# Kernel tuning notes

Hardware: AMD Instinct MI355X
Metric: run time of the kernel (lower is better)

Reference implementation:

```python
import jax, jax.numpy as jnp
import numpy as np

C = 2048
RED = 8
D = C // RED  # 256


def setup_inputs() -> dict:
    key = jax.random.key(0)
    ks = jax.random.split(key, 8)
    n, h, w = 4, 64, 64
    x = jax.random.normal(ks[0], (n, C, h, w), dtype=jnp.float32)
    # 1x1 conv weights stored as [out_ch, in_ch]
    w1 = jax.random.normal(ks[1], (D, C), dtype=jnp.float32) * 0.02
    b1 = jnp.zeros((D,), dtype=jnp.float32)
    w2 = jax.random.normal(ks[2], (D, C), dtype=jnp.float32) * 0.02
    b2 = jnp.zeros((D,), dtype=jnp.float32)
    w3 = jax.random.normal(ks[3], (C, C), dtype=jnp.float32) * 0.02
    b3 = jnp.zeros((C,), dtype=jnp.float32)
    alpha = jnp.zeros((1,), dtype=jnp.float32)
    return {"x": x, "w1": w1, "b1": b1, "w2": w2, "b2": b2,
            "w3": w3, "b3": b3, "alpha": alpha}


def reference(x, w1, b1, w2, b2, w3, b3, alpha):
    n, c, h, w = x.shape
    hw = h * w
    xf = x.reshape(n, c, hw)  # [n, C, HW]
    # 1x1 convs == per-position matmuls over channels
    e1 = jax.nn.relu(jnp.einsum('dc,ncp->ndp', w1, xf) + b1[None, :, None])  # [n, D, HW]
    e2 = jax.nn.relu(jnp.einsum('dc,ncp->ndp', w2, xf) + b2[None, :, None])  # [n, D, HW]
    assembly = jax.nn.relu(jnp.einsum('oc,ncp->nop', w3, xf) + b3[None, :, None])  # [n, C, HW]
    # attention[i, j] = softmax_j( e1[:, i] . e2[:, j] )
    scores = jnp.einsum('ndi,ndj->nij', e1, e2)  # [n, HW, HW]
    attn = jax.nn.softmax(scores, axis=-1)
    # torch.bmm(x, attn^T): out[:, :, i] = sum_j x[:, :, j] * attn[i, j]
    out = jnp.einsum('ncj,nij->nci', xf, attn)  # [n, C, HW]
    y = alpha[0] * out + assembly
    return y.reshape(n, c, h, w)
```

## Files before the change

### kernel.cpp

```cpp
#include <hip/hip_runtime.h>
#include <math.h>

#define CC 2048
#define DD 256
#define PP 4096
#define NB 4

typedef float f32x4 __attribute__((ext_vector_type(4)));
typedef __bf16 bfrag __attribute__((ext_vector_type(8)));

#define AS1(p) ((const __attribute__((address_space(1))) void*)(p))
#define AS3(p) ((__attribute__((address_space(3))) void*)(p))

__device__ __forceinline__ unsigned short f2bf(float f) {
    unsigned int u = __float_as_uint(f);
    u = (u + 0x7fffu + ((u >> 16) & 1u)) >> 16;
    return (unsigned short)u;
}

__global__ __launch_bounds__(256) void prep(const float* __restrict__ x, unsigned short* __restrict__ xT,
                                            const float* __restrict__ w3, unsigned short* __restrict__ w3b) {
    const int t = threadIdx.x;
    if (blockIdx.z == NB) {
        int bid = blockIdx.y * 64 + blockIdx.x;
        int base = (bid * 256 + t) * 8;
#pragma unroll
        for (int j = 0; j < 2; ++j) {
            float4 v = *(const float4*)(w3 + base + j * 4);
            ushort4 r;
            r.x = f2bf(v.x); r.y = f2bf(v.y); r.z = f2bf(v.z); r.w = f2bf(v.w);
            *(ushort4*)(w3b + base + j * 4) = r;
        }
        return;
    }
    __shared__ float tile[64 * 64];
    const int n  = blockIdx.z;
    const int c0 = blockIdx.y * 64;
    const int p0 = blockIdx.x * 64;
    const float* xn = x + (size_t)n * CC * PP;
    {
        const int cl = t >> 4;
        const int g  = t & 15;
        const int pl = g * 4;
#pragma unroll
        for (int ps = 0; ps < 4; ++ps) {
            const int c = cl + ps * 16;
            float4 v = *(const float4*)(xn + (size_t)(c0 + c) * PP + p0 + pl);
            const int gs = g ^ (c >> 2);
            *(float4*)(tile + c * 64 + gs * 4) = v;
        }
    }
    __syncthreads();
    unsigned short* xTn = xT + (size_t)n * PP * CC;
    {
        const int pl2 = t >> 4;
        const int cq  = t & 15;
        const int c4  = cq * 4;
#pragma unroll
        for (int ps = 0; ps < 4; ++ps) {
            const int p  = pl2 + ps * 16;
            const int gs2 = (p >> 2) ^ cq;
            const int base = gs2 * 4 + (p & 3);
            ushort4 r;
            r.x = f2bf(tile[(c4 + 0) * 64 + base]);
            r.y = f2bf(tile[(c4 + 1) * 64 + base]);
            r.z = f2bf(tile[(c4 + 2) * 64 + base]);
            r.w = f2bf(tile[(c4 + 3) * 64 + base]);
            *(ushort4*)(xTn + (size_t)(p0 + p) * CC + c0 + c4) = r;
        }
    }
}

__global__ __launch_bounds__(512, 2) void gemm_assembly(
    const unsigned short* __restrict__ w3b,
    const unsigned short* __restrict__ xT,
    const float* __restrict__ b3,
    float* __restrict__ out)
{
    __shared__ __align__(16) char sm[131072];

    const int t    = threadIdx.x;
    const int wave = t >> 6;
    const int lane = t & 63;
    const int swz  = lane & 7;

    const int p0 = blockIdx.x << 8;
    const int m0 = blockIdx.y << 8;
    const int nb = blockIdx.z;

    const int rA = t >> 3;
    const int g  = (t & 7) ^ (rA & 7);
    const unsigned short* Ag = w3b + (size_t)(m0 + rA) * CC + g * 8;
    const unsigned short* Bg = xT + (size_t)nb * PP * CC + (size_t)(p0 + rA) * CC + g * 8;
    const int ldsw = wave << 10;

    const char* Abase = sm + ((wave >> 2) << 14) + (lane & 15) * 128;
    const char* Bbase = sm + 65536 + (((wave & 3) >> 1) << 14) + ((wave & 1) << 13) + (lane & 15) * 128;

    const int ck0 = (((lane >> 4) ^ swz) << 4);
    const int ck1 = ck0 ^ 0x40;

    f32x4 acc[8][4];
#pragma unroll
    for (int i = 0; i < 8; ++i)
#pragma unroll
        for (int j = 0; j < 4; ++j)
            acc[i][j] = (f32x4){0.f, 0.f, 0.f, 0.f};

    bfrag a0k0, a0k1, a1k0, a1k1, a2k0, a2k1, a3k0, a3k1;
    bfrag a4k0, a4k1, a5k0, a5k1, a6k0, a6k1, a7k0, a7k1;
    bfrag bP0, bP1, bP2, bP3;
    bfrag bQ0, bQ1, bQ2, bQ3;

#define STG(SB, DO, kt, h) do { \
    const unsigned short* _s = (SB) + (size_t)(h) * 128 * CC + (size_t)(kt) * 64; \
    char* _d = sm + (DO) + (((kt) & 1) << 15) + ((h) << 14) + ldsw; \
    __builtin_amdgcn_global_load_lds(AS1(_s), AS3(_d), 16, 0, 0); \
    __builtin_amdgcn_global_load_lds(AS1(_s + 64 * CC), AS3(_d + 8192), 16, 0, 0); \
} while (0)

#define LD(dst, BASE, OFF) dst = *(const bfrag*)((BASE) + (OFF))
#define Q(I, J, A_, B_) acc[I][J] = __builtin_amdgcn_mfma_f32_16x16x32_bf16(A_, B_, acc[I][J], 0, 0, 0)
#define BARR __builtin_amdgcn_s_barrier()
#define SB0  __builtin_amdgcn_sched_barrier(0)
#define WLG(N) do { asm volatile("s_waitcnt lgkmcnt(" #N ")" ::: "memory"); __builtin_amdgcn_sched_barrier(0); } while (0)
#define WVM(N) asm volatile("s_waitcnt vmcnt(" #N ")" ::: "memory")
#define PRI(x) __builtin_amdgcn_s_setprio(x)

#define TILE(P, NP, kt, IA, IB, IR, V2, V0, G3, S10,S11,S12,S13, S20,S21,S22,S23) do { \
     \
    BARR; SB0; \
    LD(S20, Bbase, ((P) << 15) + (2 << 11) + ck0); LD(S21, Bbase, ((P) << 15) + (2 << 11) + ck1); \
    LD(S22, Bbase, ((P) << 15) + (3 << 11) + ck0); LD(S23, Bbase, ((P) << 15) + (3 << 11) + ck1); \
    if (IA) STG(Ag, 0, (kt) + 1, 0); \
    SB0; WLG(4); PRI(1); \
    Q(0, 0, a0k0, S10); Q(1, 0, a1k0, S10); Q(2, 0, a2k0, S10); Q(3, 0, a3k0, S10); \
    Q(0, 1, a0k0, S12); Q(1, 1, a1k0, S12); Q(2, 1, a2k0, S12); Q(3, 1, a3k0, S12); \
    Q(0, 0, a0k1, S11); Q(1, 0, a1k1, S11); Q(2, 0, a2k1, S11); Q(3, 0, a3k1, S11); \
    Q(0, 1, a0k1, S13); Q(1, 1, a1k1, S13); Q(2, 1, a2k1, S13); Q(3, 1, a3k1, S13); \
    PRI(0); \
     \
    BARR; SB0; \
    LD(a4k0, Abase, ((P) << 15) + (4 << 11) + ck0); LD(a4k1, Abase, ((P) << 15) + (4 << 11) + ck1); \
    LD(a5k0, Abase, ((P) << 15) + (5 << 11) + ck0); LD(a5k1, Abase, ((P) << 15) + (5 << 11) + ck1); \
    LD(a6k0, Abase, ((P) << 15) + (6 << 11) + ck0); LD(a6k1, Abase, ((P) << 15) + (6 << 11) + ck1); \
    LD(a7k0, Abase, ((P) << 15) + (7 << 11) + ck0); LD(a7k1, Abase, ((P) << 15) + (7 << 11) + ck1); \
    if (IA) STG(Ag, 0, (kt) + 1, 1); \
    SB0; WLG(8); PRI(1); \
    Q(0, 2, a0k0, S20); Q(1, 2, a1k0, S20); Q(2, 2, a2k0, S20); Q(3, 2, a3k0, S20); \
    Q(0, 3, a0k0, S22); Q(1, 3, a1k0, S22); Q(2, 3, a2k0, S22); Q(3, 3, a3k0, S22); \
    Q(0, 2, a0k1, S21); Q(1, 2, a1k1, S21); Q(2, 2, a2k1, S21); Q(3, 2, a3k1, S21); \
    Q(0, 3, a0k1, S23); Q(1, 3, a1k1, S23); Q(2, 3, a2k1, S23); Q(3, 3, a3k1, S23); \
    PRI(0); \
     \
     \
    BARR; SB0; \
    if (IB) STG(Bg, 65536, (kt) + 2, 0); \
    if (V2) WVM(2); \
    if (V0) WVM(0); \
    BARR; SB0; \
    if (IR) { \
        LD(a0k0, Abase, ((NP) << 15) + (0 << 11) + ck0); LD(a0k1, Abase, ((NP) << 15) + (0 << 11) + ck1); \
        LD(a1k0, Abase, ((NP) << 15) + (1 << 11) + ck0); LD(a1k1, Abase, ((NP) << 15) + (1 << 11) + ck1); \
        LD(a2k0, Abase, ((NP) << 15) + (2 << 11) + ck0); LD(a2k1, Abase, ((NP) << 15) + (2 << 11) + ck1); \
        LD(a3k0, Abase, ((NP) << 15) + (3 << 11) + ck0); LD(a3k1, Abase, ((NP) << 15) + (3 << 11) + ck1); \
    } \
    SB0; WLG(G3); PRI(1); \
    Q(4, 2, a4k0, S20); Q(5, 2, a5k0, S20); Q(6, 2, a6k0, S20); Q(7, 2, a7k0, S20); \
    Q(4, 3, a4k0, S22); Q(5, 3, a5k0, S22); Q(6, 3, a6k0, S22); Q(7, 3, a7k0, S22); \
    Q(4, 2, a4k1, S21); Q(5, 2, a5k1, S21); Q(6, 2, a6k1, S21); Q(7, 2, a7k1, S21); \
    Q(4, 3, a4k1, S23); Q(5, 3, a5k1, S23); Q(6, 3, a6k1, S23); Q(7, 3, a7k1, S23); \
    PRI(0); \
     \
    if (IB) STG(Bg, 65536, (kt) + 2, 1); \
    if (IR) { \
        LD(S20, Bbase, ((NP) << 15) + (0 << 11) + ck0); LD(S21, Bbase, ((NP) << 15) + (0 << 11) + ck1); \
        LD(S22, Bbase, ((NP) << 15) + (1 << 11) + ck0); LD(S23, Bbase, ((NP) << 15) + (1 << 11) + ck1); \
    } \
    SB0; PRI(1); \
    Q(4, 0, a4k0, S10); Q(5, 0, a5k0, S10); Q(6, 0, a6k0, S10); Q(7, 0, a7k0, S10); \
    Q(4, 1, a4k0, S12); Q(5, 1, a5k0, S12); Q(6, 1, a6k0, S12); Q(7, 1, a7k0, S12); \
    Q(4, 0, a4k1, S11); Q(5, 0, a5k1, S11); Q(6, 0, a6k1, S11); Q(7, 0, a7k1, S11); \
    Q(4, 1, a4k1, S13); Q(5, 1, a5k1, S13); Q(6, 1, a6k1, S13); Q(7, 1, a7k1, S13); \
    PRI(0); \
} while (0)

    STG(Ag, 0, 0, 0); STG(Ag, 0, 0, 1);
    STG(Bg, 65536, 0, 0); STG(Bg, 65536, 0, 1);
    STG(Bg, 65536, 1, 0); STG(Bg, 65536, 1, 1);
    WVM(4);
    BARR; SB0;
    LD(a0k0, Abase, (0 << 11) + ck0); LD(a0k1, Abase, (0 << 11) + ck1);
    LD(a1k0, Abase, (1 << 11) + ck0); LD(a1k1, Abase, (1 << 11) + ck1);
    LD(a2k0, Abase, (2 << 11) + ck0); LD(a2k1, Abase, (2 << 11) + ck1);
    LD(a3k0, Abase, (3 << 11) + ck0); LD(a3k1, Abase, (3 << 11) + ck1);
    LD(bP0, Bbase, (0 << 11) + ck0); LD(bP1, Bbase, (0 << 11) + ck1);
    LD(bP2, Bbase, (1 << 11) + ck0); LD(bP3, Bbase, (1 << 11) + ck1);
    SB0;

#pragma unroll 1
    for (int kt = 0; kt < 30; kt += 2) {
        TILE(0, 1, kt,     1, 1, 1, 1, 0, 8, bP0, bP1, bP2, bP3, bQ0, bQ1, bQ2, bQ3);
        TILE(1, 0, kt + 1, 1, 1, 1, 1, 0, 8, bQ0, bQ1, bQ2, bQ3, bP0, bP1, bP2, bP3);
    }
    TILE(0, 1, 30, 1, 0, 1, 0, 1, 8, bP0, bP1, bP2, bP3, bQ0, bQ1, bQ2, bQ3);
    TILE(1, 0, 31, 0, 0, 0, 0, 0, 0, bQ0, bQ1, bQ2, bQ3, bP0, bP1, bP2, bP3);

#undef TILE
#undef STG
#undef LD
#undef Q
#undef BARR
#undef SB0
#undef WLG
#undef WVM
#undef PRI

    const int wr = (wave >> 2) << 7;
    const int wc = (wave & 3) << 6;
    const int q4 = (lane >> 4) << 2;
    const int cl = lane & 15;
    float* outn = out + (size_t)nb * CC * PP;
#pragma unroll
    for (int mi = 0; mi < 8; ++mi) {
#pragma unroll
        for (int r = 0; r < 4; ++r) {
            const int o = m0 + wr + mi * 16 + q4 + r;
            const float bias = b3[o];
            float* orow = outn + (size_t)o * PP + p0 + wc + cl;
#pragma unroll
            for (int ni = 0; ni < 4; ++ni) {
                float v = acc[mi][ni][r] + bias;
                orow[ni * 16] = v > 0.f ? v : 0.f;
            }
        }
    }
}

__global__ void fb_e12(const float* __restrict__ x,
                       const float* __restrict__ w1, const float* __restrict__ b1,
                       const float* __restrict__ w2, const float* __restrict__ b2,
                       const float* __restrict__ alpha,
                       float* __restrict__ e1, float* __restrict__ e2) {
    if (alpha[0] == 0.f) return;
    const size_t total = (size_t)NB * DD * PP;
    for (size_t idx = (size_t)blockIdx.x * blockDim.x + threadIdx.x; idx < total;
         idx += (size_t)gridDim.x * blockDim.x) {
        int p = (int)(idx % PP);
        size_t nd = idx / PP;
        int d = (int)(nd % DD);
        int n = (int)(nd / DD);
        const float* xn = x + (size_t)n * CC * PP + p;
        float s1 = b1[d], s2 = b2[d];
        for (int c = 0; c < CC; ++c) {
            float xv = xn[(size_t)c * PP];
            s1 += w1[(size_t)d * CC + c] * xv;
            s2 += w2[(size_t)d * CC + c] * xv;
        }
        e1[idx] = fmaxf(s1, 0.f);
        e2[idx] = fmaxf(s2, 0.f);
    }
}

__global__ void fb_attn(const float* __restrict__ x,
                        const float* __restrict__ e1, const float* __restrict__ e2,
                        const float* __restrict__ alpha,
                        float* __restrict__ out) {
    const float a = alpha[0];
    if (a == 0.f) return;
    __shared__ float s[PP];
    __shared__ float e1i[DD];
    __shared__ float red[256];
    const int t = threadIdx.x;
    for (int ii = blockIdx.x; ii < NB * PP; ii += gridDim.x) {
        const int n = ii >> 12;
        const int i = ii & (PP - 1);
        const float* e1n = e1 + (size_t)n * DD * PP;
        const float* e2n = e2 + (size_t)n * DD * PP;
        if (t < DD) e1i[t] = e1n[(size_t)t * PP + i];
        __syncthreads();
        for (int j = t; j < PP; j += 256) {
            float acc = 0.f;
            for (int d = 0; d < DD; ++d) acc += e1i[d] * e2n[(size_t)d * PP + j];
            s[j] = acc;
        }
        __syncthreads();
        float m = -INFINITY;
        for (int j = t; j < PP; j += 256) m = fmaxf(m, s[j]);
        red[t] = m; __syncthreads();
        for (int o = 128; o > 0; o >>= 1) { if (t < o) red[t] = fmaxf(red[t], red[t + o]); __syncthreads(); }
        m = red[0]; __syncthreads();
        float l = 0.f;
        for (int j = t; j < PP; j += 256) { float e = __expf(s[j] - m); s[j] = e; l += e; }
        red[t] = l; __syncthreads();
        for (int o = 128; o > 0; o >>= 1) { if (t < o) red[t] += red[t + o]; __syncthreads(); }
        l = red[0]; __syncthreads();
        const float inv = a / l;
        const float* xn = x + (size_t)n * CC * PP;
        float* on = out + (size_t)n * CC * PP;
        for (int c = t; c < CC; c += 256) {
            const float* xr = xn + (size_t)c * PP;
            float acc = 0.f;
            for (int j = 0; j < PP; ++j) acc += s[j] * xr[j];
            on[(size_t)c * PP + i] += inv * acc;
        }
        __syncthreads();
    }
}

extern "C" void kernel_launch(void* const* d_in, const int* in_sizes, int n_in,
                              void* d_out, int out_size, void* d_ws, size_t ws_size,
                              hipStream_t stream) {
    (void)in_sizes; (void)n_in; (void)out_size; (void)ws_size;
    const float* x     = (const float*)d_in[0];
    const float* w1    = (const float*)d_in[1];
    const float* b1    = (const float*)d_in[2];
    const float* w2    = (const float*)d_in[3];
    const float* b2    = (const float*)d_in[4];
    const float* w3    = (const float*)d_in[5];
    const float* b3    = (const float*)d_in[6];
    const float* alpha = (const float*)d_in[7];
    float* out = (float*)d_out;

    unsigned short* xT  = (unsigned short*)d_ws;
    unsigned short* w3b = (unsigned short*)((char*)d_ws + (size_t)NB * PP * CC * 2);
    float* e1 = (float*)d_ws;
    float* e2 = e1 + (size_t)NB * DD * PP;

    prep<<<dim3(PP / 64, CC / 64, NB + 1), dim3(256), 0, stream>>>(x, xT, w3, w3b);
    gemm_assembly<<<dim3(PP / 256, CC / 256, NB), dim3(512), 0, stream>>>(w3b, xT, b3, out);
    fb_e12<<<dim3(512), dim3(256), 0, stream>>>(x, w1, b1, w2, b2, alpha, e1, e2);
    fb_attn<<<dim3(1024), dim3(256), 0, stream>>>(x, e1, e2, alpha, out);
}
```

Baseline: 360.0 us.

## Restructure GEMM tile pipeline barriers and drop ping-pong B fragment registers

Reorders the per-tile schedule in the bf16 MFMA GEMM main loop. Barriers now bracket each MFMA cluster instead of preceding each LDS-load phase, and the last quadrant's MFMAs run before the next tile's B fragments are loaded. The ping-pong B fragment register sets become one set named by column group. The aim is to cut register pressure and change how waves interleave LDS reads with MFMA work, at the cost of more barriers per tile and possibly less overlap of B loads with compute.

```diff
diff --git a/kernel.cpp b/kernel.cpp
--- a/kernel.cpp
+++ b/kernel.cpp
@@ -109,8 +109,8 @@
 
     bfrag a0k0, a0k1, a1k0, a1k1, a2k0, a2k1, a3k0, a3k1;
     bfrag a4k0, a4k1, a5k0, a5k1, a6k0, a6k1, a7k0, a7k1;
-    bfrag bP0, bP1, bP2, bP3;
-    bfrag bQ0, bQ1, bQ2, bQ3;
+    bfrag bn0k0, bn0k1, bn1k0, bn1k1;
+    bfrag bn2k0, bn2k1, bn3k0, bn3k1;
 
 #define STG(SB, DO, kt, h) do { \
     const unsigned short* _s = (SB) + (size_t)(h) * 128 * CC + (size_t)(kt) * 64; \
@@ -127,34 +127,33 @@
 #define WVM(N) asm volatile("s_waitcnt vmcnt(" #N ")" ::: "memory")
 #define PRI(x) __builtin_amdgcn_s_setprio(x)
 
-#define TILE(P, NP, kt, IA, IB, IR, V2, V0, G3, S10,S11,S12,S13, S20,S21,S22,S23) do { \
+#define TILE(P, NP, kt, IA, IB, IR, V2, V0, WL3) do { \
      \
-    BARR; SB0; \
-    LD(S20, Bbase, ((P) << 15) + (2 << 11) + ck0); LD(S21, Bbase, ((P) << 15) + (2 << 11) + ck1); \
-    LD(S22, Bbase, ((P) << 15) + (3 << 11) + ck0); LD(S23, Bbase, ((P) << 15) + (3 << 11) + ck1); \
+    SB0; \
+    LD(bn2k0, Bbase, ((P) << 15) + (2 << 11) + ck0); LD(bn2k1, Bbase, ((P) << 15) + (2 << 11) + ck1); \
+    LD(bn3k0, Bbase, ((P) << 15) + (3 << 11) + ck0); LD(bn3k1, Bbase, ((P) << 15) + (3 << 11) + ck1); \
     if (IA) STG(Ag, 0, (kt) + 1, 0); \
-    SB0; WLG(4); PRI(1); \
-    Q(0, 0, a0k0, S10); Q(1, 0, a1k0, S10); Q(2, 0, a2k0, S10); Q(3, 0, a3k0, S10); \
-    Q(0, 1, a0k0, S12); Q(1, 1, a1k0, S12); Q(2, 1, a2k0, S12); Q(3, 1, a3k0, S12); \
-    Q(0, 0, a0k1, S11); Q(1, 0, a1k1, S11); Q(2, 0, a2k1, S11); Q(3, 0, a3k1, S11); \
-    Q(0, 1, a0k1, S13); Q(1, 1, a1k1, S13); Q(2, 1, a2k1, S13); Q(3, 1, a3k1, S13); \
-    PRI(0); \
+    SB0; BARR; WLG(4); PRI(1); \
+    Q(0, 0, a0k0, bn0k0); Q(1, 0, a1k0, bn0k0); Q(2, 0, a2k0, bn0k0); Q(3, 0, a3k0, bn0k0); \
+    Q(0, 1, a0k0, bn1k0); Q(1, 1, a1k0, bn1k0); Q(2, 1, a2k0, bn1k0); Q(3, 1, a3k0, bn1k0); \
+    Q(0, 0, a0k1, bn0k1); Q(1, 0, a1k1, bn0k1); Q(2, 0, a2k1, bn0k1); Q(3, 0, a3k1, bn0k1); \
+    Q(0, 1, a0k1, bn1k1); Q(1, 1, a1k1, bn1k1); Q(2, 1, a2k1, bn1k1); Q(3, 1, a3k1, bn1k1); \
+    PRI(0); BARR; \
      \
-    BARR; SB0; \
+    SB0; \
     LD(a4k0, Abase, ((P) << 15) + (4 << 11) + ck0); LD(a4k1, Abase, ((P) << 15) + (4 << 11) + ck1); \
     LD(a5k0, Abase, ((P) << 15) + (5 << 11) + ck0); LD(a5k1, Abase, ((P) << 15) + (5 << 11) + ck1); \
     LD(a6k0, Abase, ((P) << 15) + (6 << 11) + ck0); LD(a6k1, Abase, ((P) << 15) + (6 << 11) + ck1); \
     LD(a7k0, Abase, ((P) << 15) + (7 << 11) + ck0); LD(a7k1, Abase, ((P) << 15) + (7 << 11) + ck1); \
     if (IA) STG(Ag, 0, (kt) + 1, 1); \
-    SB0; WLG(8); PRI(1); \
-    Q(0, 2, a0k0, S20); Q(1, 2, a1k0, S20); Q(2, 2, a2k0, S20); Q(3, 2, a3k0, S20); \
-    Q(0, 3, a0k0, S22); Q(1, 3, a1k0, S22); Q(2, 3, a2k0, S22); Q(3, 3, a3k0, S22); \
-    Q(0, 2, a0k1, S21); Q(1, 2, a1k1, S21); Q(2, 2, a2k1, S21); Q(3, 2, a3k1, S21); \
-    Q(0, 3, a0k1, S23); Q(1, 3, a1k1, S23); Q(2, 3, a2k1, S23); Q(3, 3, a3k1, S23); \
-    PRI(0); \
+    SB0; BARR; WLG(8); PRI(1); \
+    Q(0, 2, a0k0, bn2k0); Q(1, 2, a1k0, bn2k0); Q(2, 2, a2k0, bn2k0); Q(3, 2, a3k0, bn2k0); \
+    Q(0, 3, a0k0, bn3k0); Q(1, 3, a1k0, bn3k0); Q(2, 3, a2k0, bn3k0); Q(3, 3, a3k0, bn3k0); \
+    Q(0, 2, a0k1, bn2k1); Q(1, 2, a1k1, bn2k1); Q(2, 2, a2k1, bn2k1); Q(3, 2, a3k1, bn2k1); \
+    Q(0, 3, a0k1, bn3k1); Q(1, 3, a1k1, bn3k1); Q(2, 3, a2k1, bn3k1); Q(3, 3, a3k1, bn3k1); \
+    PRI(0); BARR; \
      \
-     \
-    BARR; SB0; \
+    SB0; \
     if (IB) STG(Bg, 65536, (kt) + 2, 0); \
     if (V2) WVM(2); \
     if (V0) WVM(0); \
@@ -165,24 +164,26 @@
         LD(a2k0, Abase, ((NP) << 15) + (2 << 11) + ck0); LD(a2k1, Abase, ((NP) << 15) + (2 << 11) + ck1); \
         LD(a3k0, Abase, ((NP) << 15) + (3 << 11) + ck0); LD(a3k1, Abase, ((NP) << 15) + (3 << 11) + ck1); \
     } \
-    SB0; WLG(G3); PRI(1); \
-    Q(4, 2, a4k0, S20); Q(5, 2, a5k0, S20); Q(6, 2, a6k0, S20); Q(7, 2, a7k0, S20); \
-    Q(4, 3, a4k0, S22); Q(5, 3, a5k0, S22); Q(6, 3, a6k0, S22); Q(7, 3, a7k0, S22); \
-    Q(4, 2, a4k1, S21); Q(5, 2, a5k1, S21); Q(6, 2, a6k1, S21); Q(7, 2, a7k1, S21); \
-    Q(4, 3, a4k1, S23); Q(5, 3, a5k1, S23); Q(6, 3, a6k1, S23); Q(7, 3, a7k1, S23); \
+    SB0; WLG(WL3); PRI(1); \
+    Q(4, 2, a4k0, bn2k0); Q(5, 2, a5k0, bn2k0); Q(6, 2, a6k0, bn2k0); Q(7, 2, a7k0, bn2k0); \
+    Q(4, 3, a4k0, bn3k0); Q(5, 3, a5k0, bn3k0); Q(6, 3, a6k0, bn3k0); Q(7, 3, a7k0, bn3k0); \
+    Q(4, 2, a4k1, bn2k1); Q(5, 2, a5k1, bn2k1); Q(6, 2, a6k1, bn2k1); Q(7, 2, a7k1, bn2k1); \
+    Q(4, 3, a4k1, bn3k1); Q(5, 3, a5k1, bn3k1); Q(6, 3, a6k1, bn3k1); Q(7, 3, a7k1, bn3k1); \
+    PRI(0); BARR; \
+     \
+    SB0; \
+    if (IB) STG(Bg, 65536, (kt) + 2, 1); \
+    SB0; BARR; SB0; PRI(1); \
+    Q(4, 0, a4k0, bn0k0); Q(5, 0, a5k0, bn0k0); Q(6, 0, a6k0, bn0k0); Q(7, 0, a7k0, bn0k0); \
+    Q(4, 1, a4k0, bn1k0); Q(5, 1, a5k0, bn1k0); Q(6, 1, a6k0, bn1k0); Q(7, 1, a7k0, bn1k0); \
+    Q(4, 0, a4k1, bn0k1); Q(5, 0, a5k1, bn0k1); Q(6, 0, a6k1, bn0k1); Q(7, 0, a7k1, bn0k1); \
+    Q(4, 1, a4k1, bn1k1); Q(5, 1, a5k1, bn1k1); Q(6, 1, a6k1, bn1k1); Q(7, 1, a7k1, bn1k1); \
     PRI(0); \
-     \
-    if (IB) STG(Bg, 65536, (kt) + 2, 1); \
     if (IR) { \
-        LD(S20, Bbase, ((NP) << 15) + (0 << 11) + ck0); LD(S21, Bbase, ((NP) << 15) + (0 << 11) + ck1); \
-        LD(S22, Bbase, ((NP) << 15) + (1 << 11) + ck0); LD(S23, Bbase, ((NP) << 15) + (1 << 11) + ck1); \
+        LD(bn0k0, Bbase, ((NP) << 15) + (0 << 11) + ck0); LD(bn0k1, Bbase, ((NP) << 15) + (0 << 11) + ck1); \
+        LD(bn1k0, Bbase, ((NP) << 15) + (1 << 11) + ck0); LD(bn1k1, Bbase, ((NP) << 15) + (1 << 11) + ck1); \
     } \
-    SB0; PRI(1); \
-    Q(4, 0, a4k0, S10); Q(5, 0, a5k0, S10); Q(6, 0, a6k0, S10); Q(7, 0, a7k0, S10); \
-    Q(4, 1, a4k0, S12); Q(5, 1, a5k0, S12); Q(6, 1, a6k0, S12); Q(7, 1, a7k0, S12); \
-    Q(4, 0, a4k1, S11); Q(5, 0, a5k1, S11); Q(6, 0, a6k1, S11); Q(7, 0, a7k1, S11); \
-    Q(4, 1, a4k1, S13); Q(5, 1, a5k1, S13); Q(6, 1, a6k1, S13); Q(7, 1, a7k1, S13); \
-    PRI(0); \
+    SB0; BARR; \
 } while (0)
 
     STG(Ag, 0, 0, 0); STG(Ag, 0, 0, 1);
@@ -194,17 +195,17 @@
     LD(a1k0, Abase, (1 << 11) + ck0); LD(a1k1, Abase, (1 << 11) + ck1);
     LD(a2k0, Abase, (2 << 11) + ck0); LD(a2k1, Abase, (2 << 11) + ck1);
     LD(a3k0, Abase, (3 << 11) + ck0); LD(a3k1, Abase, (3 << 11) + ck1);
-    LD(bP0, Bbase, (0 << 11) + ck0); LD(bP1, Bbase, (0 << 11) + ck1);
-    LD(bP2, Bbase, (1 << 11) + ck0); LD(bP3, Bbase, (1 << 11) + ck1);
+    LD(bn0k0, Bbase, (0 << 11) + ck0); LD(bn0k1, Bbase, (0 << 11) + ck1);
+    LD(bn1k0, Bbase, (1 << 11) + ck0); LD(bn1k1, Bbase, (1 << 11) + ck1);
     SB0;
 
 #pragma unroll 1
     for (int kt = 0; kt < 30; kt += 2) {
-        TILE(0, 1, kt,     1, 1, 1, 1, 0, 8, bP0, bP1, bP2, bP3, bQ0, bQ1, bQ2, bQ3);
-        TILE(1, 0, kt + 1, 1, 1, 1, 1, 0, 8, bQ0, bQ1, bQ2, bQ3, bP0, bP1, bP2, bP3);
-    }
-    TILE(0, 1, 30, 1, 0, 1, 0, 1, 8, bP0, bP1, bP2, bP3, bQ0, bQ1, bQ2, bQ3);
-    TILE(1, 0, 31, 0, 0, 0, 0, 0, 0, bQ0, bQ1, bQ2, bQ3, bP0, bP1, bP2, bP3);
+        TILE(0, 1, kt,     1, 1, 1, 1, 0, 8);
+        TILE(1, 0, kt + 1, 1, 1, 1, 1, 0, 8);
+    }
+    TILE(0, 1, 30, 1, 0, 1, 0, 1, 8);
+    TILE(1, 0, 31, 0, 0, 0, 0, 0, 0);
 
 #undef TILE
 #undef STG
```

After: 361.2 us. No clear change (+0.3%).
